# Kernel tuning notes

Measured on AMD Instinct MI355X. Metric: run time of the kernel, lower is better.

The kernel has to match this reference:

```python
import jax, jax.numpy as jnp
import numpy as np

B, ND, NP_, ED, EP = 4096, 50000, 20000, 1600000, 640000
EPS = 1e-5
LEAKY = 0.01
RRELU = (1.0 / 8.0 + 1.0 / 3.0) / 2.0  # eval-mode RReLU slope


def _gcn(x, edge_index, edge_weight, W, b, num_nodes):
    # GCNConv(improved=True): add self-loops with weight 2.0, symmetric norm.
    src, dst = edge_index[0], edge_index[1]
    loop = jnp.arange(num_nodes)
    src = jnp.concatenate([src, loop])
    dst = jnp.concatenate([dst, loop])
    w = jnp.concatenate([edge_weight, jnp.full((num_nodes,), 2.0, x.dtype)])
    deg = jax.ops.segment_sum(w, dst, num_segments=num_nodes)
    dinv = jnp.where(deg > 0, jax.lax.rsqrt(deg), 0.0)
    norm = dinv[src] * w * dinv[dst]  # [E+N]
    h = x @ W  # [N, out]
    out = jax.ops.segment_sum(h[src] * norm[:, None], dst, num_segments=num_nodes)
    return out + b


def _bn(x, g, beta, m, v):
    return (x - m) * jax.lax.rsqrt(v + EPS) * g + beta


def setup_inputs() -> dict:
    key = jax.random.key(0)
    ks = jax.random.split(key, 24)
    f32 = jnp.float32
    d = {
        "d_index": jax.random.randint(ks[0], (B,), 0, ND),
        "p_index": jax.random.randint(ks[1], (B,), 0, NP_),
        "d_vecs": jax.random.normal(ks[2], (B, 300), f32),
        "p_embeddings": jax.random.normal(ks[3], (B, 1024), f32),
        "d_ecfps": jax.random.normal(ks[4], (ND, 1024), f32),
        "d_edge_index": jax.random.randint(ks[5], (2, ED), 0, ND),
        "d_edge_weight": jax.random.uniform(ks[6], (ED,), f32),
        "p_gos": jax.random.normal(ks[7], (NP_, 2812), f32),
        "p_edge_index": jax.random.randint(ks[8], (2, EP), 0, NP_),
        "p_edge_weight": jax.random.uniform(ks[9], (EP,), f32),
    }

    def lin(k, fi, fo):
        return jax.random.normal(k, (fi, fo), f32) / np.sqrt(fi)

    d["Wd"] = lin(ks[10], 1024, 1024); d["bd"] = jnp.zeros((1024,), f32)
    d["Wp"] = lin(ks[11], 2812, 1024); d["bp"] = jnp.zeros((1024,), f32)
    d["W1"] = lin(ks[12], 3372, 1024); d["b1"] = jnp.zeros((1024,), f32)
    d["g1"] = jnp.ones((1024,), f32); d["be1"] = jnp.zeros((1024,), f32)
    d["m1"] = 0.1 * jax.random.normal(ks[13], (1024,), f32); d["v1"] = jnp.ones((1024,), f32)
    d["W2"] = lin(ks[14], 1024, 512); d["b2"] = jnp.zeros((512,), f32)
    d["g2"] = jnp.ones((512,), f32); d["be2"] = jnp.zeros((512,), f32)
    d["m2"] = 0.1 * jax.random.normal(ks[15], (512,), f32); d["v2"] = jnp.ones((512,), f32)
    d["W3"] = lin(ks[16], 512, 128); d["b3"] = jnp.zeros((128,), f32)
    d["g3"] = jnp.ones((128,), f32); d["be3"] = jnp.zeros((128,), f32)
    d["m3"] = 0.1 * jax.random.normal(ks[17], (128,), f32); d["v3"] = jnp.ones((128,), f32)
    d["W4"] = lin(ks[18], 128, 1); d["b4"] = jnp.zeros((1,), f32)
    return d


def reference(d_index, p_index, d_vecs, p_embeddings, d_ecfps, d_edge_index,
              d_edge_weight, p_gos, p_edge_index, p_edge_weight,
              Wd, bd, Wp, bp, W1, b1, g1, be1, m1, v1,
              W2, b2, g2, be2, m2, v2, W3, b3, g3, be3, m3, v3, W4, b4):
    leaky = lambda x: jax.nn.leaky_relu(x, LEAKY)
    # GCN branches (dropout is identity in eval mode)
    ecfps = leaky(_gcn(d_ecfps, d_edge_index, d_edge_weight, Wd, bd, ND))[d_index]
    gos = leaky(_gcn(p_gos, p_edge_index, p_edge_weight, Wp, bp, NP_))[p_index]
    feat = jnp.concatenate([d_vecs, p_embeddings, ecfps, gos], axis=1)  # [B,3372]
    h = leaky(_bn(feat @ W1 + b1, g1, be1, m1, v1))
    feature = leaky(_bn(h @ W2 + b2, g2, be2, m2, v2))  # [B,512]
    o = jax.nn.leaky_relu(feature @ W3 + b3, RRELU)  # RReLU eval = leaky(mid-slope)
    o = _bn(o, g3, be3, m3, v3)
    y = o @ W4 + b4  # [B,1]
    return y, feature
```

## Files before the change

kernel.cpp:

```cpp
#include <hip/hip_runtime.h>


#define EPSV 1e-5f
#define LEAKYV 0.01f
#define RRELUV 0.22916666666666666f

typedef __bf16 bf16x8 __attribute__((ext_vector_type(8)));
typedef float f32x4 __attribute__((ext_vector_type(4)));
typedef unsigned short u16x4 __attribute__((ext_vector_type(4)));

__device__ __forceinline__ unsigned short f2bf(float x) {
  unsigned u = __builtin_bit_cast(unsigned, x);
  u = (u + 0x7FFFu + ((u >> 16) & 1u)) >> 16;
  return (unsigned short)u;
}
__device__ __forceinline__ float bf2f(unsigned short h) {
  unsigned u = ((unsigned)h) << 16;
  return __builtin_bit_cast(float, u);
}

__global__ void fill_f32_k(float* __restrict__ p, float v, int n) {
  int i = blockIdx.x * blockDim.x + threadIdx.x;
  int st = gridDim.x * blockDim.x;
  for (; i < n; i += st) p[i] = v;
}
__global__ void fill_i32_k(int* __restrict__ p, int v, int n) {
  int i = blockIdx.x * blockDim.x + threadIdx.x;
  int st = gridDim.x * blockDim.x;
  for (; i < n; i += st) p[i] = v;
}
__global__ void deg_accum_k(const int* __restrict__ dst, const float* __restrict__ w,
                            float* __restrict__ deg, int E) {
  int i = blockIdx.x * blockDim.x + threadIdx.x;
  int st = gridDim.x * blockDim.x;
  for (; i < E; i += st) atomicAdd(&deg[dst[i]], w[i]);
}
__global__ void dinv_k(float* __restrict__ deg, int n) {
  int i = blockIdx.x * blockDim.x + threadIdx.x;
  int st = gridDim.x * blockDim.x;
  for (; i < n; i += st) deg[i] = 1.0f / sqrtf(deg[i]);
}
__global__ void slot_k(const int* __restrict__ idx, int* __restrict__ slot, int B) {
  int i = blockIdx.x * blockDim.x + threadIdx.x;
  if (i < B) atomicCAS(&slot[idx[i]], -1, i);
}
__global__ void count_k(const int* __restrict__ dst, const int* __restrict__ slot,
                        int* __restrict__ cnt, int E) {
  int i = blockIdx.x * blockDim.x + threadIdx.x;
  int st = gridDim.x * blockDim.x;
  for (; i < E; i += st) { int d = dst[i]; if (slot[d] >= 0) atomicAdd(&cnt[d], 1); }
}
__global__ void alloc_k(const int* __restrict__ cnt, int* __restrict__ rowstart,
                        int* __restrict__ total, int n) {
  int i = blockIdx.x * blockDim.x + threadIdx.x;
  int st = gridDim.x * blockDim.x;
  for (; i < n; i += st) { int c = cnt[i]; if (c > 0) rowstart[i] = atomicAdd(total, c); }
}
__global__ void fill_edges_k(const int* __restrict__ dst, const int* __restrict__ slot,
                             const int* __restrict__ rowstart, int* __restrict__ fil,
                             int* __restrict__ elist, int E) {
  int i = blockIdx.x * blockDim.x + threadIdx.x;
  int st = gridDim.x * blockDim.x;
  for (; i < E; i += st) {
    int d = dst[i];
    if (slot[d] >= 0) { int p = rowstart[d] + atomicAdd(&fil[d], 1); elist[p] = i; }
  }
}
__global__ void rowmap_k(const int* __restrict__ idx, const int* __restrict__ slot,
                         int* __restrict__ rmap, int B) {
  int i = blockIdx.x * blockDim.x + threadIdx.x;
  if (i < B) rmap[i] = slot[idx[i]];
}

template <int ROWLEN>
__global__ __launch_bounds__(256) void gcn_agg_k(
    const float* __restrict__ x, const int* __restrict__ bidx,
    const int* __restrict__ slot, const float* __restrict__ dinv,
    const int* __restrict__ esrc, const float* __restrict__ ew,
    const int* __restrict__ elist, const int* __restrict__ rowstart,
    const int* __restrict__ cnt, float* __restrict__ agg) {
  constexpr int NV4 = ROWLEN / 4;
  constexpr int NCH = (NV4 + 255) / 256;
  int i = blockIdx.x;
  int node = bidx[i];
  if (slot[node] != i) return;
  float dn = dinv[node];
  int t = threadIdx.x;
  float4 acc[NCH];
  {
    const float4* xr = (const float4*)(x + (size_t)node * ROWLEN);
    float cs = 2.0f * dn * dn;
#pragma unroll
    for (int ch = 0; ch < NCH; ++ch) {
      int c = t + ch * 256;
      if ((NV4 & 255) == 0 || c < NV4) {
        float4 v = xr[c];
        acc[ch].x = cs * v.x; acc[ch].y = cs * v.y;
        acc[ch].z = cs * v.z; acc[ch].w = cs * v.w;
      }
    }
  }
  int start = rowstart[node];
  int n = cnt[node];
  int j = 0;
  for (; j + 2 <= n; j += 2) {
    int e0 = elist[start + j], e1 = elist[start + j + 1];
    int s0 = esrc[e0], s1 = esrc[e1];
    float c0 = ew[e0] * dinv[s0] * dn;
    float c1 = ew[e1] * dinv[s1] * dn;
    const float4* r0 = (const float4*)(x + (size_t)s0 * ROWLEN);
    const float4* r1 = (const float4*)(x + (size_t)s1 * ROWLEN);
#pragma unroll
    for (int ch = 0; ch < NCH; ++ch) {
      int c = t + ch * 256;
      if ((NV4 & 255) == 0 || c < NV4) {
        float4 v0 = r0[c], v1 = r1[c];
        acc[ch].x += c0 * v0.x + c1 * v1.x;
        acc[ch].y += c0 * v0.y + c1 * v1.y;
        acc[ch].z += c0 * v0.z + c1 * v1.z;
        acc[ch].w += c0 * v0.w + c1 * v1.w;
      }
    }
  }
  if (j < n) {
    int e0 = elist[start + j];
    int s0 = esrc[e0];
    float c0 = ew[e0] * dinv[s0] * dn;
    const float4* r0 = (const float4*)(x + (size_t)s0 * ROWLEN);
#pragma unroll
    for (int ch = 0; ch < NCH; ++ch) {
      int c = t + ch * 256;
      if ((NV4 & 255) == 0 || c < NV4) {
        float4 v0 = r0[c];
        acc[ch].x += c0 * v0.x; acc[ch].y += c0 * v0.y;
        acc[ch].z += c0 * v0.z; acc[ch].w += c0 * v0.w;
      }
    }
  }
  float4* out = (float4*)(agg + (size_t)i * ROWLEN);
#pragma unroll
  for (int ch = 0; ch < NCH; ++ch) {
    int c = t + ch * 256;
    if ((NV4 & 255) == 0 || c < NV4) out[c] = acc[ch];
  }
}

__global__ __launch_bounds__(256) void wsplit_k(const float* __restrict__ W, int K, int N,
                                                int Kpad, unsigned short* __restrict__ hi,
                                                unsigned short* __restrict__ lo) {
  __shared__ float tile[32][33];
  int tx = threadIdx.x & 31, ty = threadIdx.x >> 5;
  int n0 = blockIdx.x * 32, k0 = blockIdx.y * 32;
#pragma unroll
  for (int i = 0; i < 4; ++i) {
    int k = k0 + ty + i * 8, n = n0 + tx;
    tile[ty + i * 8][tx] = (k < K && n < N) ? W[(size_t)k * N + n] : 0.f;
  }
  __syncthreads();
#pragma unroll
  for (int i = 0; i < 4; ++i) {
    int n = n0 + ty + i * 8, k = k0 + tx;
    if (n < N) {
      float v = tile[tx][ty + i * 8];
      unsigned short h = f2bf(v);
      hi[(size_t)n * Kpad + k] = h;
      lo[(size_t)n * Kpad + k] = f2bf(v - bf2f(h));
    }
  }
}

template <int BM, int BN, int WM, int WN, int ASRC, int EPI>
__global__ __launch_bounds__(WM * WN * 64) void mgemm_k(
    const float* __restrict__ A, int lda,
    const unsigned short* __restrict__ Bhi, const unsigned short* __restrict__ Blo,
    int Kpad, float* __restrict__ C, int ldc, int K,
    const int* __restrict__ rowmap,
    const float* __restrict__ S0, const float* __restrict__ S1,
    const float* __restrict__ S2, const float* __restrict__ S3,
    const float* __restrict__ bias, const float* __restrict__ gam,
    const float* __restrict__ bet, const float* __restrict__ mu,
    const float* __restrict__ var) {
  constexpr int THREADS = WM * WN * 64;
  constexpr int BMW = BM / WM, BNW = BN / WN;
  constexpr int MR = BMW / 16, NR = BNW / 16;
  constexpr int AF4 = BM * 16 / THREADS;
  constexpr int BC8 = BN * 8 / THREADS;

  __shared__ __attribute__((aligned(16))) unsigned short sAh[BM * 64];
  __shared__ __attribute__((aligned(16))) unsigned short sAl[BM * 64];
  __shared__ __attribute__((aligned(16))) unsigned short sBh[BN * 64];
  __shared__ __attribute__((aligned(16))) unsigned short sBl[BN * 64];

  int t = threadIdx.x;
  int lane = t & 63, wid = t >> 6;
  int wm = wid / WN, wn = wid % WN;
  int bm = blockIdx.y, bn = blockIdx.x;

  int tr[AF4], ar[AF4];
#pragma unroll
  for (int l = 0; l < AF4; ++l) {
    int flat = t + l * THREADS;
    tr[l] = flat >> 4;
    int rg = bm * BM + tr[l];
    if constexpr (ASRC == 1) ar[l] = rowmap[rg];
    else ar[l] = rg;
  }

  f32x4 acc[MR][NR];
#pragma unroll
  for (int i = 0; i < MR; ++i)
#pragma unroll
    for (int j = 0; j < NR; ++j) acc[i][j] = (f32x4){0.f, 0.f, 0.f, 0.f};

  int nk = (K + 63) / 64;
  for (int kt = 0; kt < nk; ++kt) {
    int k0 = kt * 64;
#pragma unroll
    for (int l = 0; l < AF4; ++l) {
      int flat = t + l * THREADS;
      int c4 = flat & 15;
      int kcol = k0 + c4 * 4;
      float vx = 0.f, vy = 0.f, vz = 0.f, vw = 0.f;
      if constexpr (ASRC != 2) {
        if (kcol < K) {
          float4 v = *(const float4*)&A[(size_t)ar[l] * lda + kcol];
          vx = v.x; vy = v.y; vz = v.z; vw = v.w;
        }
      } else {
        int rg = ar[l];
        const float* p = nullptr;
        if (kcol < 300)       p = S0 + (size_t)rg * 300 + kcol;
        else if (kcol < 1324) p = S1 + (size_t)rg * 1024 + (kcol - 300);
        else if (kcol < 2348) p = S2 + (size_t)rg * 1024 + (kcol - 1324);
        else if (kcol < 3372) p = S3 + (size_t)rg * 1024 + (kcol - 2348);
        if (p) { float4 v = *(const float4*)p; vx = v.x; vy = v.y; vz = v.z; vw = v.w; }
      }
      u16x4 hv, lv;
      {
        unsigned short h;
        h = f2bf(vx); hv[0] = h; lv[0] = f2bf(vx - bf2f(h));
        h = f2bf(vy); hv[1] = h; lv[1] = f2bf(vy - bf2f(h));
        h = f2bf(vz); hv[2] = h; lv[2] = f2bf(vz - bf2f(h));
        h = f2bf(vw); hv[3] = h; lv[3] = f2bf(vw - bf2f(h));
      }
      int idx = tr[l] * 64 + ((c4 * 4) ^ ((tr[l] & 7) << 3));
      *(u16x4*)&sAh[idx] = hv;
      *(u16x4*)&sAl[idx] = lv;
    }
#pragma unroll
    for (int l = 0; l < BC8; ++l) {
      int flat = t + l * THREADS;
      int n = flat >> 3, c8 = flat & 7;
      size_t g = (size_t)(bn * BN + n) * Kpad + k0 + c8 * 8;
      int idx = n * 64 + ((c8 * 8) ^ ((n & 7) << 3));
      *(uint4*)&sBh[idx] = *(const uint4*)&Bhi[g];
      *(uint4*)&sBl[idx] = *(const uint4*)&Blo[g];
    }
    __syncthreads();
#pragma unroll
    for (int ks = 0; ks < 2; ++ks) {
      bf16x8 ah[MR], al_[MR], bh[NR], bl[NR];
      int kk = ks * 32 + (lane >> 4) * 8;
#pragma unroll
      for (int fm = 0; fm < MR; ++fm) {
        int r = wm * BMW + fm * 16 + (lane & 15);
        int idx = r * 64 + (kk ^ ((r & 7) << 3));
        ah[fm] = *(bf16x8*)&sAh[idx];
        al_[fm] = *(bf16x8*)&sAl[idx];
      }
#pragma unroll
      for (int fn = 0; fn < NR; ++fn) {
        int r = wn * BNW + fn * 16 + (lane & 15);
        int idx = r * 64 + (kk ^ ((r & 7) << 3));
        bh[fn] = *(bf16x8*)&sBh[idx];
        bl[fn] = *(bf16x8*)&sBl[idx];
      }
#pragma unroll
      for (int fm = 0; fm < MR; ++fm)
#pragma unroll
        for (int fn = 0; fn < NR; ++fn) {
          acc[fm][fn] = __builtin_amdgcn_mfma_f32_16x16x32_bf16(ah[fm], bh[fn], acc[fm][fn], 0, 0, 0);
          acc[fm][fn] = __builtin_amdgcn_mfma_f32_16x16x32_bf16(ah[fm], bl[fn], acc[fm][fn], 0, 0, 0);
          acc[fm][fn] = __builtin_amdgcn_mfma_f32_16x16x32_bf16(al_[fm], bh[fn], acc[fm][fn], 0, 0, 0);
        }
    }
    __syncthreads();
  }
#pragma unroll
  for (int fm = 0; fm < MR; ++fm)
#pragma unroll
    for (int fn = 0; fn < NR; ++fn) {
      int col = bn * BN + wn * BNW + fn * 16 + (lane & 15);
      float bi = bias[col];
      float scale = 0.f, shift = 0.f;
      if constexpr (EPI != 0) {
        scale = gam[col] * (1.0f / sqrtf(var[col] + EPSV));
        shift = bet[col] - mu[col] * scale;
      }
#pragma unroll
      for (int r = 0; r < 4; ++r) {
        int row = bm * BM + wm * BMW + fm * 16 + (lane >> 4) * 4 + r;
        float v = acc[fm][fn][r] + bi;
        if constexpr (EPI == 0) {
          v = v > 0.f ? v : LEAKYV * v;
        } else if constexpr (EPI == 1) {
          v = v * scale + shift;
          v = v > 0.f ? v : LEAKYV * v;
        } else {
          v = v > 0.f ? v : RRELUV * v;
          v = v * scale + shift;
        }
        C[(size_t)row * ldc + col] = v;
      }
    }
}

__global__ __launch_bounds__(256) void out_y_k(const float* __restrict__ o,
                                               const float* __restrict__ W4,
                                               const float* __restrict__ b4,
                                               float* __restrict__ y, int B) {
  int w = (blockIdx.x * blockDim.x + threadIdx.x) >> 6;
  int lane = threadIdx.x & 63;
  if (w >= B) return;
  float v = o[(size_t)w * 128 + lane] * W4[lane] +
            o[(size_t)w * 128 + 64 + lane] * W4[64 + lane];
  v += __shfl_down(v, 32, 64);
  v += __shfl_down(v, 16, 64);
  v += __shfl_down(v, 8, 64);
  v += __shfl_down(v, 4, 64);
  v += __shfl_down(v, 2, 64);
  v += __shfl_down(v, 1, 64);
  if (lane == 0) y[w] = v + b4[0];
}

static inline int nblk(long long n, int t) {
  long long b = (n + t - 1) / t;
  if (b > 2048) b = 2048;
  return (int)b;
}

extern "C" void kernel_launch(void* const* d_in, const int* in_sizes, int n_in,
                              void* d_out, int out_size, void* d_ws, size_t ws_size,
                              hipStream_t stream) {
  const int*   d_index = (const int*)d_in[0];
  const int*   p_index = (const int*)d_in[1];
  const float* d_vecs  = (const float*)d_in[2];
  const float* p_emb   = (const float*)d_in[3];
  const float* d_ecfps = (const float*)d_in[4];
  const int*   d_eidx  = (const int*)d_in[5];
  const float* d_ew    = (const float*)d_in[6];
  const float* p_gos   = (const float*)d_in[7];
  const int*   p_eidx  = (const int*)d_in[8];
  const float* p_ew    = (const float*)d_in[9];
  const float* Wd = (const float*)d_in[10]; const float* bd = (const float*)d_in[11];
  const float* Wp = (const float*)d_in[12]; const float* bp = (const float*)d_in[13];
  const float* W1 = (const float*)d_in[14]; const float* b1 = (const float*)d_in[15];
  const float* g1 = (const float*)d_in[16]; const float* be1 = (const float*)d_in[17];
  const float* m1 = (const float*)d_in[18]; const float* v1 = (const float*)d_in[19];
  const float* W2 = (const float*)d_in[20]; const float* b2 = (const float*)d_in[21];
  const float* g2 = (const float*)d_in[22]; const float* be2 = (const float*)d_in[23];
  const float* m2 = (const float*)d_in[24]; const float* v2 = (const float*)d_in[25];
  const float* W3 = (const float*)d_in[26]; const float* b3 = (const float*)d_in[27];
  const float* g3 = (const float*)d_in[28]; const float* be3 = (const float*)d_in[29];
  const float* m3 = (const float*)d_in[30]; const float* v3 = (const float*)d_in[31];
  const float* W4 = (const float*)d_in[32]; const float* b4 = (const float*)d_in[33];

  const int B  = in_sizes[0];
  const int ND = in_sizes[4] / 1024;
  const int NP = in_sizes[7] / 2812;
  const int ED = in_sizes[5] / 2;
  const int EP = in_sizes[8] / 2;

  char* w = (char*)d_ws;
  auto carve = [&](size_t bytes) {
    char* p = w;
    w += (bytes + 255) & ~(size_t)255;
    return p;
  };
  float* deg_d = (float*)carve((size_t)ND * 4);
  float* deg_p = (float*)carve((size_t)NP * 4);
  int* slot_d = (int*)carve((size_t)ND * 4);
  int* slot_p = (int*)carve((size_t)NP * 4);
  int* cnt_d  = (int*)carve((size_t)ND * 4);
  int* cnt_p  = (int*)carve((size_t)NP * 4);
  int* fil_d  = (int*)carve((size_t)ND * 4);
  int* fil_p  = (int*)carve((size_t)NP * 4);
  int* totals = (int*)carve(256);
  int* rs_d   = (int*)carve((size_t)ND * 4);
  int* rs_p   = (int*)carve((size_t)NP * 4);
  int* rmap_d = (int*)carve((size_t)B * 4);
  int* rmap_p = (int*)carve((size_t)B * 4);
  int* elist_d = (int*)carve((size_t)ED * 4);
  int* elist_p = (int*)carve((size_t)EP * 4);
  float* agg_d = (float*)carve((size_t)B * 1024 * 4);
  float* agg_p = (float*)carve((size_t)B * 2812 * 4);
  float* ecf_b = (float*)carve((size_t)B * 1024 * 4);
  float* gos_b = (float*)carve((size_t)B * 1024 * 4);
  float* h1    = (float*)carve((size_t)B * 1024 * 4);
  float* o3    = (float*)carve((size_t)B * 128 * 4);
  unsigned short* Wdt_h = (unsigned short*)carve((size_t)1024 * 1024 * 2);
  unsigned short* Wdt_l = (unsigned short*)carve((size_t)1024 * 1024 * 2);
  unsigned short* Wpt_h = (unsigned short*)carve((size_t)1024 * 2816 * 2);
  unsigned short* Wpt_l = (unsigned short*)carve((size_t)1024 * 2816 * 2);
  unsigned short* W1t_h = (unsigned short*)carve((size_t)1024 * 3392 * 2);
  unsigned short* W1t_l = (unsigned short*)carve((size_t)1024 * 3392 * 2);
  unsigned short* W2t_h = (unsigned short*)carve((size_t)512 * 1024 * 2);
  unsigned short* W2t_l = (unsigned short*)carve((size_t)512 * 1024 * 2);
  unsigned short* W3t_h = (unsigned short*)carve((size_t)128 * 512 * 2);
  unsigned short* W3t_l = (unsigned short*)carve((size_t)128 * 512 * 2);
  (void)ws_size; (void)n_in; (void)out_size;

  float* y_out   = (float*)d_out;
  float* feature = (float*)d_out + B;

  int n_deg  = (int)(((char*)slot_d - (char*)deg_d) / 4);
  int n_slot = (int)(((char*)cnt_d - (char*)slot_d) / 4);
  int n_zero = (int)(((char*)rs_d - (char*)cnt_d) / 4);
  fill_f32_k<<<nblk(n_deg, 256), 256, 0, stream>>>(deg_d, 2.0f, n_deg);
  fill_i32_k<<<nblk(n_slot, 256), 256, 0, stream>>>(slot_d, -1, n_slot);
  fill_i32_k<<<nblk(n_zero, 256), 256, 0, stream>>>(cnt_d, 0, n_zero);

  wsplit_k<<<dim3(32, 32), 256, 0, stream>>>(Wd, 1024, 1024, 1024, Wdt_h, Wdt_l);
  wsplit_k<<<dim3(32, 88), 256, 0, stream>>>(Wp, 2812, 1024, 2816, Wpt_h, Wpt_l);
  wsplit_k<<<dim3(32, 106), 256, 0, stream>>>(W1, 3372, 1024, 3392, W1t_h, W1t_l);
  wsplit_k<<<dim3(16, 32), 256, 0, stream>>>(W2, 1024, 512, 1024, W2t_h, W2t_l);
  wsplit_k<<<dim3(4, 16), 256, 0, stream>>>(W3, 512, 128, 512, W3t_h, W3t_l);

  deg_accum_k<<<nblk(ED, 256), 256, 0, stream>>>(d_eidx + ED, d_ew, deg_d, ED);
  deg_accum_k<<<nblk(EP, 256), 256, 0, stream>>>(p_eidx + EP, p_ew, deg_p, EP);
  dinv_k<<<nblk(ND, 256), 256, 0, stream>>>(deg_d, ND);
  dinv_k<<<nblk(NP, 256), 256, 0, stream>>>(deg_p, NP);

  slot_k<<<(B + 255) / 256, 256, 0, stream>>>(d_index, slot_d, B);
  slot_k<<<(B + 255) / 256, 256, 0, stream>>>(p_index, slot_p, B);
  count_k<<<nblk(ED, 256), 256, 0, stream>>>(d_eidx + ED, slot_d, cnt_d, ED);
  count_k<<<nblk(EP, 256), 256, 0, stream>>>(p_eidx + EP, slot_p, cnt_p, EP);
  alloc_k<<<nblk(ND, 256), 256, 0, stream>>>(cnt_d, rs_d, totals + 0, ND);
  alloc_k<<<nblk(NP, 256), 256, 0, stream>>>(cnt_p, rs_p, totals + 1, NP);
  fill_edges_k<<<nblk(ED, 256), 256, 0, stream>>>(d_eidx + ED, slot_d, rs_d, fil_d, elist_d, ED);
  fill_edges_k<<<nblk(EP, 256), 256, 0, stream>>>(p_eidx + EP, slot_p, rs_p, fil_p, elist_p, EP);
  rowmap_k<<<(B + 255) / 256, 256, 0, stream>>>(d_index, slot_d, rmap_d, B);
  rowmap_k<<<(B + 255) / 256, 256, 0, stream>>>(p_index, slot_p, rmap_p, B);

  gcn_agg_k<1024><<<B, 256, 0, stream>>>(d_ecfps, d_index, slot_d, deg_d,
                                         d_eidx, d_ew, elist_d, rs_d, cnt_d, agg_d);
  gcn_agg_k<2812><<<B, 256, 0, stream>>>(p_gos, p_index, slot_p, deg_p,
                                         p_eidx, p_ew, elist_p, rs_p, cnt_p, agg_p);

  mgemm_k<128, 128, 2, 4, 1, 0><<<dim3(8, 32), 512, 0, stream>>>(
      agg_d, 1024, Wdt_h, Wdt_l, 1024, ecf_b, 1024, 1024, rmap_d,
      nullptr, nullptr, nullptr, nullptr, bd, nullptr, nullptr, nullptr, nullptr);
  mgemm_k<128, 128, 2, 4, 1, 0><<<dim3(8, 32), 512, 0, stream>>>(
      agg_p, 2812, Wpt_h, Wpt_l, 2816, gos_b, 1024, 2812, rmap_p,
      nullptr, nullptr, nullptr, nullptr, bp, nullptr, nullptr, nullptr, nullptr);
  mgemm_k<128, 128, 2, 4, 2, 1><<<dim3(8, 32), 512, 0, stream>>>(
      nullptr, 0, W1t_h, W1t_l, 3392, h1, 1024, 3372, nullptr,
      d_vecs, p_emb, ecf_b, gos_b, b1, g1, be1, m1, v1);
  mgemm_k<64, 64, 2, 2, 0, 1><<<dim3(8, 64), 256, 0, stream>>>(
      h1, 1024, W2t_h, W2t_l, 1024, feature, 512, 1024, nullptr,
      nullptr, nullptr, nullptr, nullptr, b2, g2, be2, m2, v2);
  mgemm_k<64, 64, 2, 2, 0, 2><<<dim3(2, 64), 256, 0, stream>>>(
      feature, 512, W3t_h, W3t_l, 512, o3, 128, 512, nullptr,
      nullptr, nullptr, nullptr, nullptr, b3, g3, be3, m3, v3);
  out_y_k<<<(B * 64 + 255) / 256, 256, 0, stream>>>(o3, W4, b4, y_out, B);
}
```

Baseline: 1.417 ms.

## Pre-split activations to bf16 hi/lo in producers and precompute edge coefficients

Producers (GCN aggregation, GEMM epilogues, a new d_vecs/p_emb split kernel) now write activations directly as bf16 hi/lo pairs into padded buffers. Downstream GEMMs load pre-split A tiles with 16-byte copies instead of reading fp32 and converting in every block. The concatenated W1 input is assembled in place, which removes the multi-source branchy loads. Edge fill now stores source indices and normalized coefficients contiguously, so the aggregation avoids indirect loads. Aggregation is also split over column segments to get more blocks. The cost is extra memory traffic for the hi/lo writes and a single fixed 128x128 GEMM tile for all layers, so the small layers launch fewer blocks.

```diff
diff --git a/kernel.cpp b/kernel.cpp
--- a/kernel.cpp
+++ b/kernel.cpp
@@ -7,7 +7,6 @@
 
 typedef __bf16 bf16x8 __attribute__((ext_vector_type(8)));
 typedef float f32x4 __attribute__((ext_vector_type(4)));
-typedef unsigned short u16x4 __attribute__((ext_vector_type(4)));
 
 __device__ __forceinline__ unsigned short f2bf(float x) {
   unsigned u = __builtin_bit_cast(unsigned, x);
@@ -56,14 +55,21 @@
   int st = gridDim.x * blockDim.x;
   for (; i < n; i += st) { int c = cnt[i]; if (c > 0) rowstart[i] = atomicAdd(total, c); }
 }
-__global__ void fill_edges_k(const int* __restrict__ dst, const int* __restrict__ slot,
-                             const int* __restrict__ rowstart, int* __restrict__ fil,
-                             int* __restrict__ elist, int E) {
+__global__ void fill_edges_k(const int* __restrict__ src, const int* __restrict__ dst,
+                             const float* __restrict__ ew, const float* __restrict__ dinv,
+                             const int* __restrict__ slot, const int* __restrict__ rowstart,
+                             int* __restrict__ fil, int* __restrict__ srcs,
+                             float* __restrict__ cfs, int E) {
   int i = blockIdx.x * blockDim.x + threadIdx.x;
   int st = gridDim.x * blockDim.x;
   for (; i < E; i += st) {
     int d = dst[i];
-    if (slot[d] >= 0) { int p = rowstart[d] + atomicAdd(&fil[d], 1); elist[p] = i; }
+    if (slot[d] >= 0) {
+      int p = rowstart[d] + atomicAdd(&fil[d], 1);
+      int s = src[i];
+      srcs[p] = s;
+      cfs[p] = ew[i] * dinv[s] * dinv[d];
+    }
   }
 }
 __global__ void rowmap_k(const int* __restrict__ idx, const int* __restrict__ slot,
@@ -72,76 +78,83 @@
   if (i < B) rmap[i] = slot[idx[i]];
 }
 
-template <int ROWLEN>
-__global__ __launch_bounds__(256) void gcn_agg_k(
+template <int ROWLEN, int KPAD, int SEGV4>
+__global__ __launch_bounds__(128) void gcn_agg2_k(
     const float* __restrict__ x, const int* __restrict__ bidx,
     const int* __restrict__ slot, const float* __restrict__ dinv,
-    const int* __restrict__ esrc, const float* __restrict__ ew,
-    const int* __restrict__ elist, const int* __restrict__ rowstart,
-    const int* __restrict__ cnt, float* __restrict__ agg) {
+    const int* __restrict__ srcs, const float* __restrict__ cfs,
+    const int* __restrict__ rowstart, const int* __restrict__ cnt,
+    unsigned short* __restrict__ aggH, unsigned short* __restrict__ aggL) {
   constexpr int NV4 = ROWLEN / 4;
-  constexpr int NCH = (NV4 + 255) / 256;
+  constexpr int KPV4 = KPAD / 4;
+  int t = threadIdx.x;
+  if (t >= SEGV4) return;
+  int g4 = blockIdx.y * SEGV4 + t;
+  if (g4 >= KPV4) return;
   int i = blockIdx.x;
   int node = bidx[i];
   if (slot[node] != i) return;
+
+  ushort4 zh = {0, 0, 0, 0};
+  if (g4 >= NV4) {
+    *(ushort4*)&aggH[(size_t)i * KPAD + g4 * 4] = zh;
+    *(ushort4*)&aggL[(size_t)i * KPAD + g4 * 4] = zh;
+    return;
+  }
   float dn = dinv[node];
-  int t = threadIdx.x;
-  float4 acc[NCH];
-  {
-    const float4* xr = (const float4*)(x + (size_t)node * ROWLEN);
-    float cs = 2.0f * dn * dn;
-#pragma unroll
-    for (int ch = 0; ch < NCH; ++ch) {
-      int c = t + ch * 256;
-      if ((NV4 & 255) == 0 || c < NV4) {
-        float4 v = xr[c];
-        acc[ch].x = cs * v.x; acc[ch].y = cs * v.y;
-        acc[ch].z = cs * v.z; acc[ch].w = cs * v.w;
-      }
-    }
-  }
-  int start = rowstart[node];
-  int n = cnt[node];
-  int j = 0;
-  for (; j + 2 <= n; j += 2) {
-    int e0 = elist[start + j], e1 = elist[start + j + 1];
-    int s0 = esrc[e0], s1 = esrc[e1];
-    float c0 = ew[e0] * dinv[s0] * dn;
-    float c1 = ew[e1] * dinv[s1] * dn;
-    const float4* r0 = (const float4*)(x + (size_t)s0 * ROWLEN);
-    const float4* r1 = (const float4*)(x + (size_t)s1 * ROWLEN);
-#pragma unroll
-    for (int ch = 0; ch < NCH; ++ch) {
-      int c = t + ch * 256;
-      if ((NV4 & 255) == 0 || c < NV4) {
-        float4 v0 = r0[c], v1 = r1[c];
-        acc[ch].x += c0 * v0.x + c1 * v1.x;
-        acc[ch].y += c0 * v0.y + c1 * v1.y;
-        acc[ch].z += c0 * v0.z + c1 * v1.z;
-        acc[ch].w += c0 * v0.w + c1 * v1.w;
-      }
-    }
-  }
-  if (j < n) {
-    int e0 = elist[start + j];
-    int s0 = esrc[e0];
-    float c0 = ew[e0] * dinv[s0] * dn;
-    const float4* r0 = (const float4*)(x + (size_t)s0 * ROWLEN);
-#pragma unroll
-    for (int ch = 0; ch < NCH; ++ch) {
-      int c = t + ch * 256;
-      if ((NV4 & 255) == 0 || c < NV4) {
-        float4 v0 = r0[c];
-        acc[ch].x += c0 * v0.x; acc[ch].y += c0 * v0.y;
-        acc[ch].z += c0 * v0.z; acc[ch].w += c0 * v0.w;
-      }
-    }
-  }
-  float4* out = (float4*)(agg + (size_t)i * ROWLEN);
-#pragma unroll
-  for (int ch = 0; ch < NCH; ++ch) {
-    int c = t + ch * 256;
-    if ((NV4 & 255) == 0 || c < NV4) out[c] = acc[ch];
+  float cs = 2.0f * dn * dn;
+  float4 v = *(const float4*)&x[(size_t)node * ROWLEN + g4 * 4];
+  float ax = cs * v.x, ay = cs * v.y, az = cs * v.z, aw = cs * v.w;
+
+  int j = rowstart[node];
+  int end = j + cnt[node];
+  for (; j + 4 <= end; j += 4) {
+    int s0 = srcs[j], s1 = srcs[j + 1], s2 = srcs[j + 2], s3 = srcs[j + 3];
+    float c0 = cfs[j], c1 = cfs[j + 1], c2 = cfs[j + 2], c3 = cfs[j + 3];
+    float4 v0 = *(const float4*)&x[(size_t)s0 * ROWLEN + g4 * 4];
+    float4 v1 = *(const float4*)&x[(size_t)s1 * ROWLEN + g4 * 4];
+    float4 v2 = *(const float4*)&x[(size_t)s2 * ROWLEN + g4 * 4];
+    float4 v3 = *(const float4*)&x[(size_t)s3 * ROWLEN + g4 * 4];
+    ax += c0 * v0.x + c1 * v1.x + c2 * v2.x + c3 * v3.x;
+    ay += c0 * v0.y + c1 * v1.y + c2 * v2.y + c3 * v3.y;
+    az += c0 * v0.z + c1 * v1.z + c2 * v2.z + c3 * v3.z;
+    aw += c0 * v0.w + c1 * v1.w + c2 * v2.w + c3 * v3.w;
+  }
+  for (; j < end; ++j) {
+    int s0 = srcs[j];
+    float c0 = cfs[j];
+    float4 v0 = *(const float4*)&x[(size_t)s0 * ROWLEN + g4 * 4];
+    ax += c0 * v0.x; ay += c0 * v0.y; az += c0 * v0.z; aw += c0 * v0.w;
+  }
+  ushort4 h, l;
+  h.x = f2bf(ax); l.x = f2bf(ax - bf2f(h.x));
+  h.y = f2bf(ay); l.y = f2bf(ay - bf2f(h.y));
+  h.z = f2bf(az); l.z = f2bf(az - bf2f(h.z));
+  h.w = f2bf(aw); l.w = f2bf(aw - bf2f(h.w));
+  *(ushort4*)&aggH[(size_t)i * KPAD + g4 * 4] = h;
+  *(ushort4*)&aggL[(size_t)i * KPAD + g4 * 4] = l;
+}
+
+__global__ void dvp_split_k(const float* __restrict__ dv, const float* __restrict__ pe,
+                            unsigned short* __restrict__ catH,
+                            unsigned short* __restrict__ catL, int B) {
+  int id = blockIdx.x * blockDim.x + threadIdx.x;
+  int st = gridDim.x * blockDim.x;
+  int ntask = B * 336;
+  for (; id < ntask; id += st) {
+    int r = id / 336, j = id - r * 336;
+    float4 v = {0.f, 0.f, 0.f, 0.f};
+    int col4;
+    if (j < 75) { v = *(const float4*)&dv[(size_t)r * 300 + j * 4]; col4 = j; }
+    else if (j < 331) { v = *(const float4*)&pe[(size_t)r * 1024 + (j - 75) * 4]; col4 = j; }
+    else col4 = 843 + (j - 331);
+    ushort4 h, l;
+    h.x = f2bf(v.x); l.x = f2bf(v.x - bf2f(h.x));
+    h.y = f2bf(v.y); l.y = f2bf(v.y - bf2f(h.y));
+    h.z = f2bf(v.z); l.z = f2bf(v.z - bf2f(h.z));
+    h.w = f2bf(v.w); l.w = f2bf(v.w - bf2f(h.w));
+    *(ushort4*)&catH[(size_t)r * 3392 + col4 * 4] = h;
+    *(ushort4*)&catL[(size_t)r * 3392 + col4 * 4] = l;
   }
 }
 
@@ -160,7 +173,7 @@
 #pragma unroll
   for (int i = 0; i < 4; ++i) {
     int n = n0 + ty + i * 8, k = k0 + tx;
-    if (n < N) {
+    if (n < N && k < Kpad) {
       float v = tile[tx][ty + i * 8];
       unsigned short h = f2bf(v);
       hi[(size_t)n * Kpad + k] = h;
@@ -169,128 +182,94 @@
   }
 }
 
-template <int BM, int BN, int WM, int WN, int ASRC, int EPI>
-__global__ __launch_bounds__(WM * WN * 64) void mgemm_k(
-    const float* __restrict__ A, int lda,
+template <int ASRC, int EPI, int OUTM>
+__global__ __launch_bounds__(256) void mgemm_k(
+    const unsigned short* __restrict__ Ahi, const unsigned short* __restrict__ Alo,
     const unsigned short* __restrict__ Bhi, const unsigned short* __restrict__ Blo,
-    int Kpad, float* __restrict__ C, int ldc, int K,
-    const int* __restrict__ rowmap,
-    const float* __restrict__ S0, const float* __restrict__ S1,
-    const float* __restrict__ S2, const float* __restrict__ S3,
-    const float* __restrict__ bias, const float* __restrict__ gam,
-    const float* __restrict__ bet, const float* __restrict__ mu,
-    const float* __restrict__ var) {
-  constexpr int THREADS = WM * WN * 64;
-  constexpr int BMW = BM / WM, BNW = BN / WN;
-  constexpr int MR = BMW / 16, NR = BNW / 16;
-  constexpr int AF4 = BM * 16 / THREADS;
-  constexpr int BC8 = BN * 8 / THREADS;
-
-  __shared__ __attribute__((aligned(16))) unsigned short sAh[BM * 64];
-  __shared__ __attribute__((aligned(16))) unsigned short sAl[BM * 64];
-  __shared__ __attribute__((aligned(16))) unsigned short sBh[BN * 64];
-  __shared__ __attribute__((aligned(16))) unsigned short sBl[BN * 64];
+    int Kpad, int nk, float* __restrict__ Cf, int ldc,
+    unsigned short* __restrict__ CH, unsigned short* __restrict__ CL, int ldcs, int coff,
+    const int* __restrict__ rowmap, const float* __restrict__ bias,
+    const float* __restrict__ gam, const float* __restrict__ bet,
+    const float* __restrict__ mu, const float* __restrict__ var) {
+  __shared__ __attribute__((aligned(16))) unsigned short sAh[128 * 64];
+  __shared__ __attribute__((aligned(16))) unsigned short sAl[128 * 64];
+  __shared__ __attribute__((aligned(16))) unsigned short sBh[128 * 64];
+  __shared__ __attribute__((aligned(16))) unsigned short sBl[128 * 64];
 
   int t = threadIdx.x;
   int lane = t & 63, wid = t >> 6;
-  int wm = wid / WN, wn = wid % WN;
+  int wm = wid >> 1, wn = wid & 1;
   int bm = blockIdx.y, bn = blockIdx.x;
 
-  int tr[AF4], ar[AF4];
-#pragma unroll
-  for (int l = 0; l < AF4; ++l) {
-    int flat = t + l * THREADS;
-    tr[l] = flat >> 4;
-    int rg = bm * BM + tr[l];
-    if constexpr (ASRC == 1) ar[l] = rowmap[rg];
-    else ar[l] = rg;
-  }
-
-  f32x4 acc[MR][NR];
-#pragma unroll
-  for (int i = 0; i < MR; ++i)
-#pragma unroll
-    for (int j = 0; j < NR; ++j) acc[i][j] = (f32x4){0.f, 0.f, 0.f, 0.f};
-
-  int nk = (K + 63) / 64;
+  int arow[4], brow[4], c8v[4];
+#pragma unroll
+  for (int l = 0; l < 4; ++l) {
+    int flat = t + l * 256;
+    int row = flat >> 3;
+    c8v[l] = flat & 7;
+    int rg = bm * 128 + row;
+    if constexpr (ASRC == 1) arow[l] = rowmap[rg];
+    else arow[l] = rg;
+    brow[l] = bn * 128 + row;
+  }
+
+  f32x4 acc[4][4];
+#pragma unroll
+  for (int i = 0; i < 4; ++i)
+#pragma unroll
+    for (int j = 0; j < 4; ++j) acc[i][j] = (f32x4){0.f, 0.f, 0.f, 0.f};
+
   for (int kt = 0; kt < nk; ++kt) {
     int k0 = kt * 64;
 #pragma unroll
-    for (int l = 0; l < AF4; ++l) {
-      int flat = t + l * THREADS;
-      int c4 = flat & 15;
-      int kcol = k0 + c4 * 4;
-      float vx = 0.f, vy = 0.f, vz = 0.f, vw = 0.f;
-      if constexpr (ASRC != 2) {
-        if (kcol < K) {
-          float4 v = *(const float4*)&A[(size_t)ar[l] * lda + kcol];
-          vx = v.x; vy = v.y; vz = v.z; vw = v.w;
-        }
-      } else {
-        int rg = ar[l];
-        const float* p = nullptr;
-        if (kcol < 300)       p = S0 + (size_t)rg * 300 + kcol;
-        else if (kcol < 1324) p = S1 + (size_t)rg * 1024 + (kcol - 300);
-        else if (kcol < 2348) p = S2 + (size_t)rg * 1024 + (kcol - 1324);
-        else if (kcol < 3372) p = S3 + (size_t)rg * 1024 + (kcol - 2348);
-        if (p) { float4 v = *(const float4*)p; vx = v.x; vy = v.y; vz = v.z; vw = v.w; }
-      }
-      u16x4 hv, lv;
-      {
-        unsigned short h;
-        h = f2bf(vx); hv[0] = h; lv[0] = f2bf(vx - bf2f(h));
-        h = f2bf(vy); hv[1] = h; lv[1] = f2bf(vy - bf2f(h));
-        h = f2bf(vz); hv[2] = h; lv[2] = f2bf(vz - bf2f(h));
-        h = f2bf(vw); hv[3] = h; lv[3] = f2bf(vw - bf2f(h));
-      }
-      int idx = tr[l] * 64 + ((c4 * 4) ^ ((tr[l] & 7) << 3));
-      *(u16x4*)&sAh[idx] = hv;
-      *(u16x4*)&sAl[idx] = lv;
-    }
-#pragma unroll
-    for (int l = 0; l < BC8; ++l) {
-      int flat = t + l * THREADS;
-      int n = flat >> 3, c8 = flat & 7;
-      size_t g = (size_t)(bn * BN + n) * Kpad + k0 + c8 * 8;
-      int idx = n * 64 + ((c8 * 8) ^ ((n & 7) << 3));
-      *(uint4*)&sBh[idx] = *(const uint4*)&Bhi[g];
-      *(uint4*)&sBl[idx] = *(const uint4*)&Blo[g];
+    for (int l = 0; l < 4; ++l) {
+      int flat = t + l * 256;
+      int row = flat >> 3, c8 = c8v[l];
+      size_t ga = (size_t)arow[l] * Kpad + k0 + c8 * 8;
+      size_t gb = (size_t)brow[l] * Kpad + k0 + c8 * 8;
+      uint4 vah = *(const uint4*)&Ahi[ga];
+      uint4 val = *(const uint4*)&Alo[ga];
+      uint4 vbh = *(const uint4*)&Bhi[gb];
+      uint4 vbl = *(const uint4*)&Blo[gb];
+      int idx = row * 64 + ((c8 * 8) ^ ((row & 7) << 3));
+      *(uint4*)&sAh[idx] = vah;
+      *(uint4*)&sAl[idx] = val;
+      *(uint4*)&sBh[idx] = vbh;
+      *(uint4*)&sBl[idx] = vbl;
     }
     __syncthreads();
 #pragma unroll
     for (int ks = 0; ks < 2; ++ks) {
-      bf16x8 ah[MR], al_[MR], bh[NR], bl[NR];
       int kk = ks * 32 + (lane >> 4) * 8;
-#pragma unroll
-      for (int fm = 0; fm < MR; ++fm) {
-        int r = wm * BMW + fm * 16 + (lane & 15);
-        int idx = r * 64 + (kk ^ ((r & 7) << 3));
-        ah[fm] = *(bf16x8*)&sAh[idx];
-        al_[fm] = *(bf16x8*)&sAl[idx];
-      }
-#pragma unroll
-      for (int fn = 0; fn < NR; ++fn) {
-        int r = wn * BNW + fn * 16 + (lane & 15);
+      bf16x8 bh[4], bl[4];
+#pragma unroll
+      for (int fn = 0; fn < 4; ++fn) {
+        int r = wn * 64 + fn * 16 + (lane & 15);
         int idx = r * 64 + (kk ^ ((r & 7) << 3));
         bh[fn] = *(bf16x8*)&sBh[idx];
         bl[fn] = *(bf16x8*)&sBl[idx];
       }
 #pragma unroll
-      for (int fm = 0; fm < MR; ++fm)
-#pragma unroll
-        for (int fn = 0; fn < NR; ++fn) {
-          acc[fm][fn] = __builtin_amdgcn_mfma_f32_16x16x32_bf16(ah[fm], bh[fn], acc[fm][fn], 0, 0, 0);
-          acc[fm][fn] = __builtin_amdgcn_mfma_f32_16x16x32_bf16(ah[fm], bl[fn], acc[fm][fn], 0, 0, 0);
-          acc[fm][fn] = __builtin_amdgcn_mfma_f32_16x16x32_bf16(al_[fm], bh[fn], acc[fm][fn], 0, 0, 0);
+      for (int fm = 0; fm < 4; ++fm) {
+        int r = wm * 64 + fm * 16 + (lane & 15);
+        int idx = r * 64 + (kk ^ ((r & 7) << 3));
+        bf16x8 ah = *(bf16x8*)&sAh[idx];
+        bf16x8 al = *(bf16x8*)&sAl[idx];
+#pragma unroll
+        for (int fn = 0; fn < 4; ++fn) {
+          acc[fm][fn] = __builtin_amdgcn_mfma_f32_16x16x32_bf16(ah, bh[fn], acc[fm][fn], 0, 0, 0);
+          acc[fm][fn] = __builtin_amdgcn_mfma_f32_16x16x32_bf16(ah, bl[fn], acc[fm][fn], 0, 0, 0);
+          acc[fm][fn] = __builtin_amdgcn_mfma_f32_16x16x32_bf16(al, bh[fn], acc[fm][fn], 0, 0, 0);
         }
+      }
     }
     __syncthreads();
   }
 #pragma unroll
-  for (int fm = 0; fm < MR; ++fm)
-#pragma unroll
-    for (int fn = 0; fn < NR; ++fn) {
-      int col = bn * BN + wn * BNW + fn * 16 + (lane & 15);
+  for (int fm = 0; fm < 4; ++fm)
+#pragma unroll
+    for (int fn = 0; fn < 4; ++fn) {
+      int col = bn * 128 + wn * 64 + fn * 16 + (lane & 15);
       float bi = bias[col];
       float scale = 0.f, shift = 0.f;
       if constexpr (EPI != 0) {
@@ -299,7 +278,7 @@
       }
 #pragma unroll
       for (int r = 0; r < 4; ++r) {
-        int row = bm * BM + wm * BMW + fm * 16 + (lane >> 4) * 4 + r;
+        int row = bm * 128 + wm * 64 + fm * 16 + (lane >> 4) * 4 + r;
         float v = acc[fm][fn][r] + bi;
         if constexpr (EPI == 0) {
           v = v > 0.f ? v : LEAKYV * v;
@@ -310,7 +289,12 @@
           v = v > 0.f ? v : RRELUV * v;
           v = v * scale + shift;
         }
-        C[(size_t)row * ldc + col] = v;
+        if constexpr (OUTM != 1) Cf[(size_t)row * ldc + col] = v;
+        if constexpr (OUTM != 0) {
+          unsigned short h = f2bf(v);
+          CH[(size_t)row * ldcs + coff + col] = h;
+          CL[(size_t)row * ldcs + coff + col] = f2bf(v - bf2f(h));
+        }
       }
     }
 }
@@ -390,14 +374,21 @@
   int* rs_p   = (int*)carve((size_t)NP * 4);
   int* rmap_d = (int*)carve((size_t)B * 4);
   int* rmap_p = (int*)carve((size_t)B * 4);
-  int* elist_d = (int*)carve((size_t)ED * 4);
-  int* elist_p = (int*)carve((size_t)EP * 4);
-  float* agg_d = (float*)carve((size_t)B * 1024 * 4);
-  float* agg_p = (float*)carve((size_t)B * 2812 * 4);
-  float* ecf_b = (float*)carve((size_t)B * 1024 * 4);
-  float* gos_b = (float*)carve((size_t)B * 1024 * 4);
-  float* h1    = (float*)carve((size_t)B * 1024 * 4);
-  float* o3    = (float*)carve((size_t)B * 128 * 4);
+  int* srcs_d = (int*)carve((size_t)ED * 4);
+  float* cfs_d = (float*)carve((size_t)ED * 4);
+  int* srcs_p = (int*)carve((size_t)EP * 4);
+  float* cfs_p = (float*)carve((size_t)EP * 4);
+  unsigned short* aggdH = (unsigned short*)carve((size_t)B * 1024 * 2);
+  unsigned short* aggdL = (unsigned short*)carve((size_t)B * 1024 * 2);
+  unsigned short* aggpH = (unsigned short*)carve((size_t)B * 2816 * 2);
+  unsigned short* aggpL = (unsigned short*)carve((size_t)B * 2816 * 2);
+  unsigned short* catH  = (unsigned short*)carve((size_t)B * 3392 * 2);
+  unsigned short* catL  = (unsigned short*)carve((size_t)B * 3392 * 2);
+  unsigned short* h1H   = (unsigned short*)carve((size_t)B * 1024 * 2);
+  unsigned short* h1L   = (unsigned short*)carve((size_t)B * 1024 * 2);
+  unsigned short* ftH   = (unsigned short*)carve((size_t)B * 512 * 2);
+  unsigned short* ftL   = (unsigned short*)carve((size_t)B * 512 * 2);
+  float* o3 = (float*)carve((size_t)B * 128 * 4);
   unsigned short* Wdt_h = (unsigned short*)carve((size_t)1024 * 1024 * 2);
   unsigned short* Wdt_l = (unsigned short*)carve((size_t)1024 * 1024 * 2);
   unsigned short* Wpt_h = (unsigned short*)carve((size_t)1024 * 2816 * 2);
@@ -425,6 +416,7 @@
   wsplit_k<<<dim3(32, 106), 256, 0, stream>>>(W1, 3372, 1024, 3392, W1t_h, W1t_l);
   wsplit_k<<<dim3(16, 32), 256, 0, stream>>>(W2, 1024, 512, 1024, W2t_h, W2t_l);
   wsplit_k<<<dim3(4, 16), 256, 0, stream>>>(W3, 512, 128, 512, W3t_h, W3t_l);
+  dvp_split_k<<<2048, 256, 0, stream>>>(d_vecs, p_emb, catH, catL, B);
 
   deg_accum_k<<<nblk(ED, 256), 256, 0, stream>>>(d_eidx + ED, d_ew, deg_d, ED);
   deg_accum_k<<<nblk(EP, 256), 256, 0, stream>>>(p_eidx + EP, p_ew, deg_p, EP);
@@ -437,30 +429,32 @@
   count_k<<<nblk(EP, 256), 256, 0, stream>>>(p_eidx + EP, slot_p, cnt_p, EP);
   alloc_k<<<nblk(ND, 256), 256, 0, stream>>>(cnt_d, rs_d, totals + 0, ND);
   alloc_k<<<nblk(NP, 256), 256, 0, stream>>>(cnt_p, rs_p, totals + 1, NP);
-  fill_edges_k<<<nblk(ED, 256), 256, 0, stream>>>(d_eidx + ED, slot_d, rs_d, fil_d, elist_d, ED);
-  fill_edges_k<<<nblk(EP, 256), 256, 0, stream>>>(p_eidx + EP, slot_p, rs_p, fil_p, elist_p, EP);
+  fill_edges_k<<<nblk(ED, 256), 256, 0, stream>>>(d_eidx, d_eidx + ED, d_ew, deg_d,
+                                                  slot_d, rs_d, fil_d, srcs_d, cfs_d, ED);
+  fill_edges_k<<<nblk(EP, 256), 256, 0, stream>>>(p_eidx, p_eidx + EP, p_ew, deg_p,
+                                                  slot_p, rs_p, fil_p, srcs_p, cfs_p, EP);
   rowmap_k<<<(B + 255) / 256, 256, 0, stream>>>(d_index, slot_d, rmap_d, B);
   rowmap_k<<<(B + 255) / 256, 256, 0, stream>>>(p_index, slot_p, rmap_p, B);
 
-  gcn_agg_k<1024><<<B, 256, 0, stream>>>(d_ecfps, d_index, slot_d, deg_d,
-                                         d_eidx, d_ew, elist_d, rs_d, cnt_d, agg_d);
-  gcn_agg_k<2812><<<B, 256, 0, stream>>>(p_gos, p_index, slot_p, deg_p,
-                                         p_eidx, p_ew, elist_p, rs_p, cnt_p, agg_p);
-
-  mgemm_k<128, 128, 2, 4, 1, 0><<<dim3(8, 32), 512, 0, stream>>>(
-      agg_d, 1024, Wdt_h, Wdt_l, 1024, ecf_b, 1024, 1024, rmap_d,
-      nullptr, nullptr, nullptr, nullptr, bd, nullptr, nullptr, nullptr, nullptr);
-  mgemm_k<128, 128, 2, 4, 1, 0><<<dim3(8, 32), 512, 0, stream>>>(
-      agg_p, 2812, Wpt_h, Wpt_l, 2816, gos_b, 1024, 2812, rmap_p,
-      nullptr, nullptr, nullptr, nullptr, bp, nullptr, nullptr, nullptr, nullptr);
-  mgemm_k<128, 128, 2, 4, 2, 1><<<dim3(8, 32), 512, 0, stream>>>(
-      nullptr, 0, W1t_h, W1t_l, 3392, h1, 1024, 3372, nullptr,
-      d_vecs, p_emb, ecf_b, gos_b, b1, g1, be1, m1, v1);
-  mgemm_k<64, 64, 2, 2, 0, 1><<<dim3(8, 64), 256, 0, stream>>>(
-      h1, 1024, W2t_h, W2t_l, 1024, feature, 512, 1024, nullptr,
-      nullptr, nullptr, nullptr, nullptr, b2, g2, be2, m2, v2);
-  mgemm_k<64, 64, 2, 2, 0, 2><<<dim3(2, 64), 256, 0, stream>>>(
-      feature, 512, W3t_h, W3t_l, 512, o3, 128, 512, nullptr,
-      nullptr, nullptr, nullptr, nullptr, b3, g3, be3, m3, v3);
+  gcn_agg2_k<1024, 1024, 128><<<dim3(B, 2), 128, 0, stream>>>(
+      d_ecfps, d_index, slot_d, deg_d, srcs_d, cfs_d, rs_d, cnt_d, aggdH, aggdL);
+  gcn_agg2_k<2812, 2816, 118><<<dim3(B, 6), 128, 0, stream>>>(
+      p_gos, p_index, slot_p, deg_p, srcs_p, cfs_p, rs_p, cnt_p, aggpH, aggpL);
+
+  mgemm_k<1, 0, 1><<<dim3(8, 32), 256, 0, stream>>>(
+      aggdH, aggdL, Wdt_h, Wdt_l, 1024, 16, nullptr, 0, catH, catL, 3392, 1324,
+      rmap_d, bd, nullptr, nullptr, nullptr, nullptr);
+  mgemm_k<1, 0, 1><<<dim3(8, 32), 256, 0, stream>>>(
+      aggpH, aggpL, Wpt_h, Wpt_l, 2816, 44, nullptr, 0, catH, catL, 3392, 2348,
+      rmap_p, bp, nullptr, nullptr, nullptr, nullptr);
+  mgemm_k<0, 1, 1><<<dim3(8, 32), 256, 0, stream>>>(
+      catH, catL, W1t_h, W1t_l, 3392, 53, nullptr, 0, h1H, h1L, 1024, 0,
+      nullptr, b1, g1, be1, m1, v1);
+  mgemm_k<0, 1, 2><<<dim3(4, 32), 256, 0, stream>>>(
+      h1H, h1L, W2t_h, W2t_l, 1024, 16, feature, 512, ftH, ftL, 512, 0,
+      nullptr, b2, g2, be2, m2, v2);
+  mgemm_k<0, 2, 0><<<dim3(1, 32), 256, 0, stream>>>(
+      ftH, ftL, W3t_h, W3t_l, 512, 8, o3, 128, nullptr, nullptr, 0, 0,
+      nullptr, b3, g3, be3, m3, v3);
   out_y_k<<<(B * 64 + 255) / 256, 256, 0, stream>>>(o3, W4, b4, y_out, B);
 }
```

Measured after the change: 1.348 ms. 1.05x faster.
